# Kernel optimization log

Measured on AMD Instinct MI355X. Metric: run time of the kernel, lower is better.

## Reference

```python
import jax, jax.numpy as jnp
import numpy as np

B, D, M, C = 256, 256, 65536, 1000
TEMP = 0.05
ALPHA_WEIGHT = 0.5
EPS = 1e-6


def setup_inputs() -> dict:
    key = jax.random.key(0)
    k = jax.random.split(key, 6)
    feat = jax.random.normal(k[0], (B, D), dtype=jnp.float32)
    features = jax.random.normal(k[1], (M, D), dtype=jnp.float32)
    features = features / jnp.clip(jnp.linalg.norm(features, axis=1, keepdims=True), 1e-12)
    sample_softlabels = jax.random.uniform(k[2], (M, C), dtype=jnp.float32)
    indexes = jax.random.randint(k[3], (B,), 0, M, dtype=jnp.int32)
    labels = jax.random.randint(k[4], (M,), 0, C, dtype=jnp.int32)
    batch_indexs_labels = jax.random.randint(k[5], (B,), 0, M, dtype=jnp.int32)
    return {
        "feat": feat,
        "features": features,
        "sample_softlabels": sample_softlabels,
        "indexes": indexes,
        "labels": labels,
        "batch_indexs_labels": batch_indexs_labels,
        "cur_epoch": 1,
    }


def reference(feat, features, sample_softlabels, indexes, labels, batch_indexs_labels, cur_epoch):
    # L2-normalize batch features (F.normalize with eps clamp)
    x = feat / jnp.clip(jnp.linalg.norm(feat, axis=1, keepdims=True), 1e-12)
    # HM.apply forward: similarity vs memory bank (memory momentum update is a
    # buffer side-effect and does not affect the returned loss)
    logits = (x @ features.T) / TEMP  # [B, M]
    # group similarities by class label of each memory slot (index_add_)
    sim = jax.ops.segment_sum(logits.T, labels, num_segments=C)  # [C, B]
    nums = jax.ops.segment_sum(jnp.ones((M,), jnp.float32), labels, num_segments=C)  # [C]
    mask = nums > 0
    sim = sim / jnp.where(mask, nums, 1.0)[:, None]  # class-mean similarity [C, B]
    simT = sim.T  # [B, C]
    # masked softmax over classes
    exps = jnp.exp(simT) * mask[None, :].astype(simT.dtype)
    probs = exps / (jnp.sum(exps, axis=1, keepdims=True) + EPS)
    log_probs = jnp.log(probs + EPS)  # [B, C]
    targets = labels[indexes]  # [B]
    loss1 = -jnp.mean(log_probs[jnp.arange(B), targets])
    if cur_epoch == 0:
        return loss1
    batch_soft_labels = sample_softlabels[batch_indexs_labels]  # [B, C]
    loss2 = jnp.sum(jnp.mean(-batch_soft_labels * log_probs, axis=0))
    return ALPHA_WEIGHT * loss1 + (1.0 - ALPHA_WEIGHT) * loss2
```

## Files before the change

### kernel.cpp

```cpp
#include <hip/hip_runtime.h>

#define B_SZ 256
#define D_SZ 256
#define M_SZ 65536
#define C_SZ 1000
#define TEMP 0.05f
#define EPSF 1e-6f

#define CPB 4
#define NBLK_CSUM (C_SZ / CPB)
#define LCAP 512

#define OFF_FCT   0
#define OFF_NUMS  1024000
#define OFF_ACC   1028000
#define OFF_LCNT  1028008

__launch_bounds__(1024)
__global__ void k_csum(const float* __restrict__ features,
                       const int* __restrict__ labels,
                       float* __restrict__ fct, int* __restrict__ nums,
                       float* __restrict__ acc, int* __restrict__ lcnt) {
    __shared__ int list[CPB][LCAP];
    __shared__ int lcur[CPB];
    int t = threadIdx.x, b = blockIdx.x;
    int c0 = b * CPB;

    if (t < CPB) lcur[t] = 0;
    if (b == 0 && t == 0) { acc[0] = 0.f; acc[1] = 0.f; lcnt[0] = 0; }
    __syncthreads();

    const int4* L4 = (const int4*)labels;
    #pragma unroll
    for (int k = 0; k < M_SZ / 4 / 1024; ++k) {
        int idx = k * 1024 + t;
        int4 l4 = L4[idx];
        int m0 = idx * 4;
        unsigned d;
        d = (unsigned)(l4.x - c0); if (d < CPB) list[d][atomicAdd(&lcur[d], 1)] = m0 + 0;
        d = (unsigned)(l4.y - c0); if (d < CPB) list[d][atomicAdd(&lcur[d], 1)] = m0 + 1;
        d = (unsigned)(l4.z - c0); if (d < CPB) list[d][atomicAdd(&lcur[d], 1)] = m0 + 2;
        d = (unsigned)(l4.w - c0); if (d < CPB) list[d][atomicAdd(&lcur[d], 1)] = m0 + 3;
    }
    __syncthreads();

    int g = t >> 8, tt = t & 255;
    int c = c0 + g;
    int n = lcur[g];
    const int* ml = list[g];
    float a0 = 0.f, a1 = 0.f, a2 = 0.f, a3 = 0.f;
    float a4 = 0.f, a5 = 0.f, a6 = 0.f, a7 = 0.f;
    int i = 0;
    for (; i + 8 <= n; i += 8) {
        int r0 = ml[i + 0];
        int r1 = ml[i + 1];
        int r2 = ml[i + 2];
        int r3 = ml[i + 3];
        int r4 = ml[i + 4];
        int r5 = ml[i + 5];
        int r6 = ml[i + 6];
        int r7 = ml[i + 7];
        a0 += features[(size_t)r0 * D_SZ + tt];
        a1 += features[(size_t)r1 * D_SZ + tt];
        a2 += features[(size_t)r2 * D_SZ + tt];
        a3 += features[(size_t)r3 * D_SZ + tt];
        a4 += features[(size_t)r4 * D_SZ + tt];
        a5 += features[(size_t)r5 * D_SZ + tt];
        a6 += features[(size_t)r6 * D_SZ + tt];
        a7 += features[(size_t)r7 * D_SZ + tt];
    }
    for (; i < n; ++i) a0 += features[(size_t)ml[i] * D_SZ + tt];
    float s = ((a0 + a1) + (a2 + a3)) + ((a4 + a5) + (a6 + a7));
    float scale = 1.0f / (TEMP * (float)(n > 0 ? n : 1));
    fct[(size_t)tt * C_SZ + c] = s * scale;
    if (tt == 0) nums[c] = n;
}

__launch_bounds__(1024)
__global__ void k_loss(const float* __restrict__ feat,
                       const float* __restrict__ fct,
                       const int* __restrict__ nums,
                       const float* __restrict__ soft,
                       const int* __restrict__ indexes,
                       const int* __restrict__ labels,
                       const int* __restrict__ bil,
                       const int* __restrict__ cur_epoch,
                       float* __restrict__ acc, int* __restrict__ lcnt,
                       float* __restrict__ out) {
    __shared__ float xs0[D_SZ], xs1[D_SZ];
    __shared__ float wred[16], wred2[16];
    __shared__ float bc0, bc1;
    __shared__ int tgt0, tgt1, sr0, sr1;

    int t = threadIdx.x;
    int lane = t & 63, wid = t >> 6;
    int r0 = blockIdx.x * 2;

    if (t == 0) {
        tgt0 = labels[indexes[r0]];
        tgt1 = labels[indexes[r0 + 1]];
        sr0 = bil[r0];
        sr1 = bil[r0 + 1];
    }

    float v = (t < 512) ? feat[(size_t)r0 * D_SZ + t] : 0.f;
    float s = v * v;
    #pragma unroll
    for (int o = 32; o; o >>= 1) s += __shfl_down(s, o);
    if (lane == 0) wred[wid] = s;
    __syncthreads();
    if (t == 0) {
        bc0 = fmaxf(sqrtf(wred[0] + wred[1] + wred[2] + wred[3]), 1e-12f);
        bc1 = fmaxf(sqrtf(wred[4] + wred[5] + wred[6] + wred[7]), 1e-12f);
    }
    __syncthreads();
    if (t < 256) xs0[t] = v / bc0;
    else if (t < 512) xs1[t - 256] = v / bc1;
    __syncthreads();

    float a0 = 0.f, a1 = 0.f;
    if (t < C_SZ) {
        #pragma unroll 8
        for (int i = 0; i < D_SZ; ++i) {
            float f = fct[(size_t)i * C_SZ + t];
            a0 = fmaf(xs0[i], f, a0);
            a1 = fmaf(xs1[i], f, a1);
        }
    }
    float mk = (t < C_SZ && nums[t] > 0) ? 1.f : 0.f;
    float e0 = mk * __expf(a0);
    float e1 = mk * __expf(a1);

    float s0 = e0, s1 = e1;
    #pragma unroll
    for (int o = 32; o; o >>= 1) {
        s0 += __shfl_down(s0, o);
        s1 += __shfl_down(s1, o);
    }
    if (lane == 0) { wred[wid] = s0; wred2[wid] = s1; }
    __syncthreads();
    if (t == 0) {
        float z0 = 0.f, z1 = 0.f;
        #pragma unroll
        for (int i = 0; i < 16; ++i) { z0 += wred[i]; z1 += wred2[i]; }
        bc0 = z0; bc1 = z1;
    }
    __syncthreads();
    float inv0 = 1.0f / (bc0 + EPSF);
    float inv1 = 1.0f / (bc1 + EPSF);

    float p1 = 0.f, p2 = 0.f;
    if (t < C_SZ) {
        float lp0 = __logf(e0 * inv0 + EPSF);
        float lp1 = __logf(e1 * inv1 + EPSF);
        p2 = -(soft[(size_t)sr0 * C_SZ + t] * lp0 + soft[(size_t)sr1 * C_SZ + t] * lp1);
        if (t == tgt0) p1 -= lp0;
        if (t == tgt1) p1 -= lp1;
    }
    #pragma unroll
    for (int o = 32; o; o >>= 1) {
        p1 += __shfl_down(p1, o);
        p2 += __shfl_down(p2, o);
    }
    __syncthreads();
    if (lane == 0) { wred[wid] = p1; wred2[wid] = p2; }
    __syncthreads();
    if (t == 0) {
        float z1 = 0.f, z2 = 0.f;
        #pragma unroll
        for (int i = 0; i < 16; ++i) { z1 += wred[i]; z2 += wred2[i]; }
        atomicAdd(&acc[0], z1);
        atomicAdd(&acc[1], z2);
        __threadfence();
        int done = atomicAdd(lcnt, 1);
        if (done == (int)gridDim.x - 1) {
            float l1 = atomicAdd(&acc[0], 0.f) / (float)B_SZ;
            float l2 = atomicAdd(&acc[1], 0.f) / (float)B_SZ;
            out[0] = (cur_epoch[0] == 0) ? l1 : 0.5f * (l1 + l2);
        }
    }
}

extern "C" void kernel_launch(void* const* d_in, const int* in_sizes, int n_in,
                              void* d_out, int out_size, void* d_ws, size_t ws_size,
                              hipStream_t stream) {
    const float* feat     = (const float*)d_in[0];
    const float* features = (const float*)d_in[1];
    const float* soft     = (const float*)d_in[2];
    const int* indexes    = (const int*)d_in[3];
    const int* labels     = (const int*)d_in[4];
    const int* bil        = (const int*)d_in[5];
    const int* cur_epoch  = (const int*)d_in[6];

    char* ws = (char*)d_ws;
    float* fct   = (float*)(ws + OFF_FCT);
    int* nums    = (int*)(ws + OFF_NUMS);
    float* acc   = (float*)(ws + OFF_ACC);
    int* lcnt    = (int*)(ws + OFF_LCNT);

    k_csum<<<NBLK_CSUM, 1024, 0, stream>>>(features, labels, fct, nums, acc, lcnt);
    k_loss<<<B_SZ / 2, 1024, 0, stream>>>(feat, fct, nums, soft, indexes, labels,
                                          bil, cur_epoch, acc, lcnt, (float*)d_out);
}
```

Baseline: 49.18 us.

## Vectorize class-sum gather with float4 and interleave centroid layout by four dims

The class-sum kernel now handles 2 classes per block. Each class gets 512 threads arranged as 8 row-slices of 64 lanes, and each lane loads a float4 of a feature row. A shared-memory reduction combines the slices. The centroid table is stored as float4 groups of four dimensions per class, so the loss kernel can read float4 values and cut its global load count by four. This doubles the csum block count and adds a shared reduction and sync. It also requires the fct layout change to stay consistent between the two kernels.

```diff
diff --git a/kernel.cpp b/kernel.cpp
--- a/kernel.cpp
+++ b/kernel.cpp
@@ -7,9 +7,10 @@
 #define TEMP 0.05f
 #define EPSF 1e-6f
 
-#define CPB 4
+#define CPB 2
 #define NBLK_CSUM (C_SZ / CPB)
 #define LCAP 512
+
 
 #define OFF_FCT   0
 #define OFF_NUMS  1024000
@@ -23,6 +24,7 @@
                        float* __restrict__ acc, int* __restrict__ lcnt) {
     __shared__ int list[CPB][LCAP];
     __shared__ int lcur[CPB];
+    __shared__ float4 red[CPB][8][64];
     int t = threadIdx.x, b = blockIdx.x;
     int c0 = b * CPB;
 
@@ -44,36 +46,33 @@
     }
     __syncthreads();
 
-    int g = t >> 8, tt = t & 255;
+    int g = t >> 9;
+    int tt = t & 511;
+    int s = tt >> 6;
+    int lane = tt & 63;
     int c = c0 + g;
     int n = lcur[g];
     const int* ml = list[g];
-    float a0 = 0.f, a1 = 0.f, a2 = 0.f, a3 = 0.f;
-    float a4 = 0.f, a5 = 0.f, a6 = 0.f, a7 = 0.f;
-    int i = 0;
-    for (; i + 8 <= n; i += 8) {
-        int r0 = ml[i + 0];
-        int r1 = ml[i + 1];
-        int r2 = ml[i + 2];
-        int r3 = ml[i + 3];
-        int r4 = ml[i + 4];
-        int r5 = ml[i + 5];
-        int r6 = ml[i + 6];
-        int r7 = ml[i + 7];
-        a0 += features[(size_t)r0 * D_SZ + tt];
-        a1 += features[(size_t)r1 * D_SZ + tt];
-        a2 += features[(size_t)r2 * D_SZ + tt];
-        a3 += features[(size_t)r3 * D_SZ + tt];
-        a4 += features[(size_t)r4 * D_SZ + tt];
-        a5 += features[(size_t)r5 * D_SZ + tt];
-        a6 += features[(size_t)r6 * D_SZ + tt];
-        a7 += features[(size_t)r7 * D_SZ + tt];
-    }
-    for (; i < n; ++i) a0 += features[(size_t)ml[i] * D_SZ + tt];
-    float s = ((a0 + a1) + (a2 + a3)) + ((a4 + a5) + (a6 + a7));
-    float scale = 1.0f / (TEMP * (float)(n > 0 ? n : 1));
-    fct[(size_t)tt * C_SZ + c] = s * scale;
-    if (tt == 0) nums[c] = n;
+    float4 a = make_float4(0.f, 0.f, 0.f, 0.f);
+    #pragma unroll 2
+    for (int i = s; i < n; i += 8) {
+        float4 v = *(const float4*)&features[(size_t)ml[i] * D_SZ + lane * 4];
+        a.x += v.x; a.y += v.y; a.z += v.z; a.w += v.w;
+    }
+    red[g][s][lane] = a;
+    __syncthreads();
+    if (s == 0) {
+        float4 z = make_float4(0.f, 0.f, 0.f, 0.f);
+        #pragma unroll
+        for (int q = 0; q < 8; ++q) {
+            float4 r = red[g][q][lane];
+            z.x += r.x; z.y += r.y; z.z += r.z; z.w += r.w;
+        }
+        float scale = 1.0f / (TEMP * (float)(n > 0 ? n : 1));
+        z.x *= scale; z.y *= scale; z.z *= scale; z.w *= scale;
+        *(float4*)&fct[(size_t)lane * (C_SZ * 4) + c * 4] = z;
+        if (lane == 0) nums[c] = n;
+    }
 }
 
 __launch_bounds__(1024)
@@ -120,11 +119,16 @@
 
     float a0 = 0.f, a1 = 0.f;
     if (t < C_SZ) {
-        #pragma unroll 8
-        for (int i = 0; i < D_SZ; ++i) {
-            float f = fct[(size_t)i * C_SZ + t];
-            a0 = fmaf(xs0[i], f, a0);
-            a1 = fmaf(xs1[i], f, a1);
+        const float4* F = (const float4*)fct;
+        #pragma unroll 4
+        for (int j = 0; j < D_SZ / 4; ++j) {
+            float4 f4 = F[(size_t)j * C_SZ + t];
+            float4 x0 = *(const float4*)&xs0[4 * j];
+            float4 x1 = *(const float4*)&xs1[4 * j];
+            a0 = fmaf(x0.x, f4.x, a0); a0 = fmaf(x0.y, f4.y, a0);
+            a0 = fmaf(x0.z, f4.z, a0); a0 = fmaf(x0.w, f4.w, a0);
+            a1 = fmaf(x1.x, f4.x, a1); a1 = fmaf(x1.y, f4.y, a1);
+            a1 = fmaf(x1.z, f4.z, a1); a1 = fmaf(x1.w, f4.w, a1);
         }
     }
     float mk = (t < C_SZ && nums[t] > 0) ? 1.f : 0.f;
```

After: 41.41 us. 1.19x faster.
